# Performance work log

Hardware: AMD Instinct MI355X
Metric: run time of the kernel (lower is better)

Reference implementation:

```python
import jax, jax.numpy as jnp
import numpy as np

SEQ, B, I, H = 512, 64, 1024, 1024

def setup_inputs() -> dict:
    key = jax.random.key(0)
    ks = jax.random.split(key, 6)
    scale_ih = 1.0 / np.sqrt(I)
    scale_hh = 1.0 / np.sqrt(H)
    return {
        "input": jax.random.normal(ks[0], (SEQ, B, I), dtype=jnp.float32),
        "h_0": jax.random.normal(ks[1], (1, B, H), dtype=jnp.float32),
        "weight_ih": jax.random.normal(ks[2], (3 * H, I), dtype=jnp.float32) * scale_ih,
        "weight_hh": jax.random.normal(ks[3], (3 * H, H), dtype=jnp.float32) * scale_hh,
        "bias_ih": jax.random.normal(ks[4], (3 * H,), dtype=jnp.float32) * scale_hh,
        "bias_hh": jax.random.normal(ks[5], (3 * H,), dtype=jnp.float32) * scale_hh,
    }


def _gru_lbr0(input, h0, weight_ih, weight_hh, bias_ih, bias_hh):
    """Unidirectional GRU, ONNX linear_before_reset=0 semantics.

    r_t = sigmoid(x W_ir^T + b_ir + h W_hr^T + b_hr)
    z_t = sigmoid(x W_iz^T + b_iz + h W_hz^T + b_hz)
    n_t = tanh(x W_in^T + b_in + (r_t * h) W_hn^T + b_hn)
    h_t = (1 - z_t) * n_t + z_t * h
    """
    hidden = h0.shape[-1]
    # Precompute all input projections in one big GEMM: (S, B, 3H)
    gx = jnp.einsum('sbi,gi->sbg', input, weight_ih) + bias_ih
    W_hr, W_hz, W_hn = jnp.split(weight_hh, 3, axis=0)
    b_hr, b_hz, b_hn = jnp.split(bias_hh, 3, axis=0)

    def step(h, gx_t):
        gx_r, gx_z, gx_n = jnp.split(gx_t, 3, axis=-1)
        r = jax.nn.sigmoid(gx_r + h @ W_hr.T + b_hr)
        z = jax.nn.sigmoid(gx_z + h @ W_hz.T + b_hz)
        n = jnp.tanh(gx_n + (r * h) @ W_hn.T + b_hn)
        h_new = (1.0 - z) * n + z * h
        return h_new, h_new

    h_n, outputs = jax.lax.scan(step, h0, gx)
    return outputs, h_n  # (S, B, H), (B, H)


def reference(input, h_0, weight_ih, weight_hh, bias_ih, bias_hh):
    seq_len, batch, _ = input.shape
    hidden = weight_hh.shape[1]
    outputs, h_n = _gru_lbr0(input, h_0[0], weight_ih, weight_hh, bias_ih, bias_hh)
    # Match GRUWrapper output layout: Y = (S, num_dir=1, B, H), Y_h = (1, B, H)
    Y = outputs.reshape(seq_len, batch, 1, hidden).transpose(0, 2, 1, 3)
    Y_h = h_n[None, :, :]
    return (Y, Y_h)
```

## Files before the change

kernel.cpp:

```cpp
#include <hip/hip_runtime.h>

typedef unsigned short ushort_t;
typedef short sh8 __attribute__((ext_vector_type(8)));
typedef float f32x4 __attribute__((ext_vector_type(4)));

#define MFMA16(a,b,c) __builtin_amdgcn_mfma_f32_16x16x32_bf16((a),(b),(c),0,0,0)

#define SEQL   512
#define BATCH  64
#define HDIM   1024
#define G3     3072
#define AROWS  (SEQL*BATCH)
#define YSZ    (SEQL*BATCH*HDIM)
#define BH     (BATCH*HDIM)
#define NWG    64

__device__ __forceinline__ ushort_t f2bf(float x) {
  unsigned u = __float_as_uint(x);
  u += 0x7FFFu + ((u >> 16) & 1u);
  return (ushort_t)(u >> 16);
}
__device__ __forceinline__ float bf2f(ushort_t h) {
  return __uint_as_float(((unsigned)h) << 16);
}

__global__ void cvt_kernel(const float* __restrict__ wih, const float* __restrict__ whh,
                           const float* __restrict__ h0,
                           ushort_t* __restrict__ WihH, ushort_t* __restrict__ WihL,
                           ushort_t* __restrict__ WhhH, ushort_t* __restrict__ WhhL,
                           ushort_t* __restrict__ hH) {
  const int NW = G3 * HDIM;
  int i0 = blockIdx.x * blockDim.x + threadIdx.x;
  int stride = gridDim.x * blockDim.x;
  for (int i = i0; i < NW; i += stride) {
    float x = wih[i]; ushort_t h = f2bf(x);
    WihH[i] = h; WihL[i] = f2bf(x - bf2f(h));
    float y = whh[i]; ushort_t g = f2bf(y);
    WhhH[i] = g; WhhL[i] = f2bf(y - bf2f(g));
  }
  for (int i = i0; i < BH; i += stride) {
    hH[i] = f2bf(h0[i]);
  }
}

__global__ __launch_bounds__(256) void gemm_gx(
    const float* __restrict__ A,
    const ushort_t* __restrict__ BHp, const ushort_t* __restrict__ BLp,
    const float* __restrict__ bias,
    float* __restrict__ gx)
{
  int bid = blockIdx.x;
  int mt = bid / 24, nt = bid % 24;
  int w = threadIdx.x >> 6, l = threadIdx.x & 63;
  int lr = l & 15, lk = (l >> 4) * 8;

  f32x4 acc[2][8];
  #pragma unroll
  for (int mi = 0; mi < 2; ++mi)
    #pragma unroll
    for (int ni = 0; ni < 8; ++ni) acc[mi][ni] = (f32x4){0.f, 0.f, 0.f, 0.f};

  int arow0 = mt * 128 + w * 32 + lr;
  int brow0 = nt * 128 + lr;

  for (int k0 = 0; k0 < HDIM; k0 += 32) {
    int ka = k0 + lk;
    sh8 aH[2], aL[2];
    #pragma unroll
    for (int mi = 0; mi < 2; ++mi) {
      const float* ap = A + (size_t)(arow0 + mi * 16) * HDIM + ka;
      float4 x0 = *(const float4*)ap;
      float4 x1 = *(const float4*)(ap + 4);
      float xs[8] = {x0.x, x0.y, x0.z, x0.w, x1.x, x1.y, x1.z, x1.w};
      #pragma unroll
      for (int j = 0; j < 8; ++j) {
        ushort_t h = f2bf(xs[j]);
        aH[mi][j] = (short)h;
        aL[mi][j] = (short)f2bf(xs[j] - bf2f(h));
      }
    }
    #pragma unroll
    for (int ni = 0; ni < 8; ++ni) {
      const ushort_t* bh = BHp + (size_t)(brow0 + ni * 16) * HDIM + ka;
      const ushort_t* bl = BLp + (size_t)(brow0 + ni * 16) * HDIM + ka;
      sh8 bHf = *(const sh8*)bh;
      sh8 bLf = *(const sh8*)bl;
      #pragma unroll
      for (int mi = 0; mi < 2; ++mi) {
        acc[mi][ni] = MFMA16(aH[mi], bHf, acc[mi][ni]);
        acc[mi][ni] = MFMA16(aH[mi], bLf, acc[mi][ni]);
        acc[mi][ni] = MFMA16(aL[mi], bHf, acc[mi][ni]);
      }
    }
  }
  int rb = (l >> 4) * 4;
  #pragma unroll
  for (int mi = 0; mi < 2; ++mi)
    #pragma unroll
    for (int ni = 0; ni < 8; ++ni) {
      int col = nt * 128 + ni * 16 + lr;
      float b = bias[col];
      #pragma unroll
      for (int j = 0; j < 4; ++j) {
        int row = mt * 128 + w * 32 + mi * 16 + rb + j;
        __builtin_nontemporal_store(acc[mi][ni][j] + b, &gx[(size_t)row * G3 + col]);
      }
    }
}

__device__ __forceinline__ void gbar_flat(unsigned* slots, int g, int tid, unsigned e) {
  __syncthreads();
  if (tid < 64) {
    if (tid == 0)
      __hip_atomic_store(slots + g * 32, e, __ATOMIC_RELEASE, __HIP_MEMORY_SCOPE_AGENT);
    unsigned* sp = slots + tid * 32;
    while (__hip_atomic_load(sp, __ATOMIC_RELAXED, __HIP_MEMORY_SCOPE_AGENT) < e)
      __builtin_amdgcn_s_sleep(1);
    (void)__hip_atomic_load(sp, __ATOMIC_ACQUIRE, __HIP_MEMORY_SCOPE_AGENT);
  }
  __syncthreads();
}

__global__ __launch_bounds__(256, 1) void gru_rec(
    const float* __restrict__ gx,
    const ushort_t* __restrict__ WhhH, const ushort_t* __restrict__ WhhL,
    const float* __restrict__ bias_hh,
    const float* __restrict__ h0f,
    ushort_t* __restrict__ hH,
    ushort_t* __restrict__ rhH,
    float* __restrict__ Y, float* __restrict__ Yh,
    unsigned* __restrict__ slots)
{
  extern __shared__ char lds[];
  const int g = blockIdx.x;
  const int tid = threadIdx.x;
  const int w = tid >> 6, l = tid & 63;
  const int lr = l & 15, lk = (l >> 4) * 8, rb = (l >> 4) * 4;
  const int c0 = g * 16, m0 = w * 16;
  const int c = c0 + lr;

  #pragma unroll
  for (int p = 0; p < 32; ++p) {
    int q = tid + p * 256;
    int flat = q * 16;
    int lrow = flat >> 11;
    int off = flat & 2047;
    int dst = flat ^ ((lrow & 7) << 4);
    const ushort_t* src;
    if (lrow < 16)      src = WhhH + (size_t)(c0 + lrow) * HDIM;
    else if (lrow < 32) src = WhhH + (size_t)(1024 + c0 + lrow - 16) * HDIM;
    else if (lrow < 48) src = WhhH + (size_t)(2048 + c0 + lrow - 32) * HDIM;
    else                src = WhhL + (size_t)(2048 + c0 + lrow - 48) * HDIM;
    *(sh8*)(lds + dst) = *(const sh8*)(src + (off >> 1));
  }
  __syncthreads();

  const float br = bias_hh[c], bz = bias_hh[1024 + c], bn = bias_hh[2048 + c];
  unsigned bar = 0;

  float hold[4];
  #pragma unroll
  for (int j = 0; j < 4; ++j) hold[j] = h0f[(m0 + rb + j) * HDIM + c];

  float gxr[4], gxz[4], gxn[4];
  #pragma unroll
  for (int j = 0; j < 4; ++j) {
    int b = m0 + rb + j;
    gxr[j] = __builtin_nontemporal_load(gx + (size_t)b * G3 + c);
    gxz[j] = __builtin_nontemporal_load(gx + (size_t)b * G3 + 1024 + c);
    gxn[j] = __builtin_nontemporal_load(gx + (size_t)b * G3 + 2048 + c);
  }

  for (int t = 0; t < SEQL; ++t) {
    const int par = t & 1;

    const ushort_t* ha = hH + par * BH + (size_t)(m0 + lr) * HDIM + lk;
    sh8 bufa[32];
    #pragma unroll
    for (int i = 0; i < 32; ++i) bufa[i] = *(const sh8*)(ha + i * 32);

    f32x4 accR = (f32x4){0,0,0,0}, accZ = (f32x4){0,0,0,0};
    #pragma unroll
    for (int i = 0; i < 32; ++i) {
      int byt = ((lr << 11) + ((i * 32 + lk) << 1)) ^ ((lr & 7) << 4);
      sh8 rW = *(const sh8*)(lds + byt);
      sh8 zW = *(const sh8*)(lds + 32768 + byt);
      accR = MFMA16(bufa[i], rW, accR);
      accZ = MFMA16(bufa[i], zW, accZ);
    }

    float zreg[4];
    #pragma unroll
    for (int j = 0; j < 4; ++j) {
      int b = m0 + rb + j;
      float pr = accR[j] + gxr[j] + br;
      float pz = accZ[j] + gxz[j] + bz;
      float r = 1.f / (1.f + __expf(-pr));
      zreg[j] = 1.f / (1.f + __expf(-pz));
      rhH[b * HDIM + c] = f2bf(r * hold[j]);
    }
    ++bar;
    gbar_flat(slots, g, tid, bar);

    const ushort_t* ra = rhH + (size_t)(m0 + lr) * HDIM + lk;
    #pragma unroll
    for (int i = 0; i < 32; ++i) bufa[i] = *(const sh8*)(ra + i * 32);

    {
      int tn = (t + 1 < SEQL) ? t + 1 : t;
      const float* gxn2 = gx + (size_t)tn * (BATCH * G3);
      #pragma unroll
      for (int j = 0; j < 4; ++j) {
        int b = m0 + rb + j;
        gxr[j] = __builtin_nontemporal_load(gxn2 + (size_t)b * G3 + c);
        gxz[j] = __builtin_nontemporal_load(gxn2 + (size_t)b * G3 + 1024 + c);
      }
    }

    f32x4 accN = (f32x4){0,0,0,0};
    #pragma unroll
    for (int i = 0; i < 32; ++i) {
      int byt = ((lr << 11) + ((i * 32 + lk) << 1)) ^ ((lr & 7) << 4);
      sh8 nW = *(const sh8*)(lds + 65536 + byt);
      sh8 nLo = *(const sh8*)(lds + 98304 + byt);
      accN = MFMA16(bufa[i], nW, accN);
      accN = MFMA16(bufa[i], nLo, accN);
    }

    ushort_t* hHn = hH + (par ^ 1) * BH;
    float gxnN[4];
    {
      int tn = (t + 1 < SEQL) ? t + 1 : t;
      const float* gxn2 = gx + (size_t)tn * (BATCH * G3);
      #pragma unroll
      for (int j = 0; j < 4; ++j) {
        int b = m0 + rb + j;
        gxnN[j] = __builtin_nontemporal_load(gxn2 + (size_t)b * G3 + 2048 + c);
      }
    }
    #pragma unroll
    for (int j = 0; j < 4; ++j) {
      int b = m0 + rb + j;
      float pn = accN[j] + gxn[j] + bn;
      float n = tanhf(pn);
      float z = zreg[j];
      float hnew = (1.f - z) * n + z * hold[j];
      hold[j] = hnew;
      __builtin_nontemporal_store(hnew, &Y[(size_t)t * BH + b * HDIM + c]);
      hHn[b * HDIM + c] = f2bf(hnew);
      if (t == SEQL - 1) __builtin_nontemporal_store(hnew, &Yh[b * HDIM + c]);
    }
    #pragma unroll
    for (int j = 0; j < 4; ++j) gxn[j] = gxnN[j];

    if (t < SEQL - 1) {
      ++bar;
      gbar_flat(slots, g, tid, bar);
    }
  }
}

extern "C" void kernel_launch(void* const* d_in, const int* in_sizes, int n_in,
                              void* d_out, int out_size, void* d_ws, size_t ws_size,
                              hipStream_t stream) {
  const float* input = (const float*)d_in[0];
  const float* h0    = (const float*)d_in[1];
  const float* wih   = (const float*)d_in[2];
  const float* whh   = (const float*)d_in[3];
  const float* bih   = (const float*)d_in[4];
  const float* bhh   = (const float*)d_in[5];

  char* ws = (char*)d_ws;
  size_t o = 0;
  float* gx = (float*)(ws + o);         o += (size_t)AROWS * G3 * 4;
  ushort_t* WihH = (ushort_t*)(ws + o); o += (size_t)G3 * HDIM * 2;
  ushort_t* WihL = (ushort_t*)(ws + o); o += (size_t)G3 * HDIM * 2;
  ushort_t* WhhH = (ushort_t*)(ws + o); o += (size_t)G3 * HDIM * 2;
  ushort_t* WhhL = (ushort_t*)(ws + o); o += (size_t)G3 * HDIM * 2;
  ushort_t* hH = (ushort_t*)(ws + o);   o += 2 * (size_t)BH * 2;
  ushort_t* rhH = (ushort_t*)(ws + o);  o += (size_t)BH * 2;
  unsigned* slots = (unsigned*)(ws + o); o += (size_t)NWG * 128;

  float* Y  = (float*)d_out;
  float* Yh = (float*)d_out + (size_t)YSZ;

  (void)hipFuncSetAttribute((const void*)gru_rec,
                            hipFuncAttributeMaxDynamicSharedMemorySize, 131072);

  (void)hipMemsetAsync(slots, 0, (size_t)NWG * 128, stream);
  cvt_kernel<<<2048, 256, 0, stream>>>(wih, whh, h0, WihH, WihL, WhhH, WhhL, hH);
  gemm_gx<<<(AROWS / 128) * (G3 / 128), 256, 0, stream>>>(input, WihH, WihL, bih, gx);
  gru_rec<<<64, 256, 131072, stream>>>(gx, WhhH, WhhL, bhh, h0, hH, rhH, Y, Yh, slots);
}
```

Measured before the change: 8.765 ms.

## Replace acquire/release barrier with relaxed atomics on 32-bit-padded hidden state

```diff
diff --git a/kernel.cpp b/kernel.cpp
--- a/kernel.cpp
+++ b/kernel.cpp
@@ -28,7 +28,7 @@
                            const float* __restrict__ h0,
                            ushort_t* __restrict__ WihH, ushort_t* __restrict__ WihL,
                            ushort_t* __restrict__ WhhH, ushort_t* __restrict__ WhhL,
-                           ushort_t* __restrict__ hH) {
+                           unsigned* __restrict__ hU) {
   const int NW = G3 * HDIM;
   int i0 = blockIdx.x * blockDim.x + threadIdx.x;
   int stride = gridDim.x * blockDim.x;
@@ -39,7 +39,7 @@
     WhhH[i] = g; WhhL[i] = f2bf(y - bf2f(g));
   }
   for (int i = i0; i < BH; i += stride) {
-    hH[i] = f2bf(h0[i]);
+    hU[i] = (unsigned)f2bf(h0[i]);
   }
 }
 
@@ -108,28 +108,40 @@
     }
 }
 
-__device__ __forceinline__ void gbar_flat(unsigned* slots, int g, int tid, unsigned e) {
+__device__ __forceinline__ void gbar_nf(unsigned* slots, int g, int tid, unsigned e) {
   __syncthreads();
   if (tid < 64) {
     if (tid == 0)
-      __hip_atomic_store(slots + g * 32, e, __ATOMIC_RELEASE, __HIP_MEMORY_SCOPE_AGENT);
-    unsigned* sp = slots + tid * 32;
-    while (__hip_atomic_load(sp, __ATOMIC_RELAXED, __HIP_MEMORY_SCOPE_AGENT) < e)
+      __hip_atomic_store(slots + g, e, __ATOMIC_RELAXED, __HIP_MEMORY_SCOPE_AGENT);
+    while (__hip_atomic_load(slots + tid, __ATOMIC_RELAXED, __HIP_MEMORY_SCOPE_AGENT) < e)
       __builtin_amdgcn_s_sleep(1);
-    (void)__hip_atomic_load(sp, __ATOMIC_ACQUIRE, __HIP_MEMORY_SCOPE_AGENT);
   }
   __syncthreads();
 }
+
+#define LOADU(BUF_, base_) \
+  _Pragma("unroll") for (int i = 0; i < 32; ++i) { \
+    unsigned long long* p = (unsigned long long*)((base_) + i * 32); \
+    unsigned long long q0 = __hip_atomic_load(p + 0, __ATOMIC_RELAXED, __HIP_MEMORY_SCOPE_AGENT); \
+    unsigned long long q1 = __hip_atomic_load(p + 1, __ATOMIC_RELAXED, __HIP_MEMORY_SCOPE_AGENT); \
+    unsigned long long q2 = __hip_atomic_load(p + 2, __ATOMIC_RELAXED, __HIP_MEMORY_SCOPE_AGENT); \
+    unsigned long long q3 = __hip_atomic_load(p + 3, __ATOMIC_RELAXED, __HIP_MEMORY_SCOPE_AGENT); \
+    union { unsigned u[4]; sh8 s; } f_; \
+    f_.u[0] = (unsigned)q0 | ((unsigned)(q0 >> 32) << 16); \
+    f_.u[1] = (unsigned)q1 | ((unsigned)(q1 >> 32) << 16); \
+    f_.u[2] = (unsigned)q2 | ((unsigned)(q2 >> 32) << 16); \
+    f_.u[3] = (unsigned)q3 | ((unsigned)(q3 >> 32) << 16); \
+    BUF_[i] = f_.s; }
 
 __global__ __launch_bounds__(256, 1) void gru_rec(
     const float* __restrict__ gx,
     const ushort_t* __restrict__ WhhH, const ushort_t* __restrict__ WhhL,
     const float* __restrict__ bias_hh,
     const float* __restrict__ h0f,
-    ushort_t* __restrict__ hH,
-    ushort_t* __restrict__ rhH,
+    unsigned* hU,
+    unsigned* rhU,
     float* __restrict__ Y, float* __restrict__ Yh,
-    unsigned* __restrict__ slots)
+    unsigned* slots)
 {
   extern __shared__ char lds[];
   const int g = blockIdx.x;
@@ -174,10 +186,9 @@
   for (int t = 0; t < SEQL; ++t) {
     const int par = t & 1;
 
-    const ushort_t* ha = hH + par * BH + (size_t)(m0 + lr) * HDIM + lk;
+    unsigned* ha = hU + par * BH + (m0 + lr) * HDIM + lk;
     sh8 bufa[32];
-    #pragma unroll
-    for (int i = 0; i < 32; ++i) bufa[i] = *(const sh8*)(ha + i * 32);
+    LOADU(bufa, ha)
 
     f32x4 accR = (f32x4){0,0,0,0}, accZ = (f32x4){0,0,0,0};
     #pragma unroll
@@ -197,23 +208,23 @@
       float pz = accZ[j] + gxz[j] + bz;
       float r = 1.f / (1.f + __expf(-pr));
       zreg[j] = 1.f / (1.f + __expf(-pz));
-      rhH[b * HDIM + c] = f2bf(r * hold[j]);
+      __hip_atomic_store(rhU + b * HDIM + c, (unsigned)f2bf(r * hold[j]),
+                         __ATOMIC_RELAXED, __HIP_MEMORY_SCOPE_AGENT);
     }
     ++bar;
-    gbar_flat(slots, g, tid, bar);
-
-    const ushort_t* ra = rhH + (size_t)(m0 + lr) * HDIM + lk;
-    #pragma unroll
-    for (int i = 0; i < 32; ++i) bufa[i] = *(const sh8*)(ra + i * 32);
+    gbar_nf(slots, g, tid, bar);
+
+    unsigned* ra = rhU + (m0 + lr) * HDIM + lk;
+    LOADU(bufa, ra)
 
     {
       int tn = (t + 1 < SEQL) ? t + 1 : t;
-      const float* gxn2 = gx + (size_t)tn * (BATCH * G3);
+      const float* gxt1 = gx + (size_t)tn * (BATCH * G3);
       #pragma unroll
       for (int j = 0; j < 4; ++j) {
         int b = m0 + rb + j;
-        gxr[j] = __builtin_nontemporal_load(gxn2 + (size_t)b * G3 + c);
-        gxz[j] = __builtin_nontemporal_load(gxn2 + (size_t)b * G3 + 1024 + c);
+        gxr[j] = __builtin_nontemporal_load(gxt1 + (size_t)b * G3 + c);
+        gxz[j] = __builtin_nontemporal_load(gxt1 + (size_t)b * G3 + 1024 + c);
       }
     }
 
@@ -227,17 +238,18 @@
       accN = MFMA16(bufa[i], nLo, accN);
     }
 
-    ushort_t* hHn = hH + (par ^ 1) * BH;
     float gxnN[4];
     {
       int tn = (t + 1 < SEQL) ? t + 1 : t;
-      const float* gxn2 = gx + (size_t)tn * (BATCH * G3);
+      const float* gxt1 = gx + (size_t)tn * (BATCH * G3);
       #pragma unroll
       for (int j = 0; j < 4; ++j) {
         int b = m0 + rb + j;
-        gxnN[j] = __builtin_nontemporal_load(gxn2 + (size_t)b * G3 + 2048 + c);
-      }
-    }
+        gxnN[j] = __builtin_nontemporal_load(gxt1 + (size_t)b * G3 + 2048 + c);
+      }
+    }
+
+    unsigned* hUn = hU + (par ^ 1) * BH;
     #pragma unroll
     for (int j = 0; j < 4; ++j) {
       int b = m0 + rb + j;
@@ -246,16 +258,17 @@
       float z = zreg[j];
       float hnew = (1.f - z) * n + z * hold[j];
       hold[j] = hnew;
-      __builtin_nontemporal_store(hnew, &Y[(size_t)t * BH + b * HDIM + c]);
-      hHn[b * HDIM + c] = f2bf(hnew);
-      if (t == SEQL - 1) __builtin_nontemporal_store(hnew, &Yh[b * HDIM + c]);
+      Y[(size_t)t * BH + b * HDIM + c] = hnew;
+      __hip_atomic_store(hUn + b * HDIM + c, (unsigned)f2bf(hnew),
+                         __ATOMIC_RELAXED, __HIP_MEMORY_SCOPE_AGENT);
+      if (t == SEQL - 1) Yh[b * HDIM + c] = hnew;
     }
     #pragma unroll
     for (int j = 0; j < 4; ++j) gxn[j] = gxnN[j];
 
     if (t < SEQL - 1) {
       ++bar;
-      gbar_flat(slots, g, tid, bar);
+      gbar_nf(slots, g, tid, bar);
     }
   }
 }
@@ -277,9 +290,9 @@
   ushort_t* WihL = (ushort_t*)(ws + o); o += (size_t)G3 * HDIM * 2;
   ushort_t* WhhH = (ushort_t*)(ws + o); o += (size_t)G3 * HDIM * 2;
   ushort_t* WhhL = (ushort_t*)(ws + o); o += (size_t)G3 * HDIM * 2;
-  ushort_t* hH = (ushort_t*)(ws + o);   o += 2 * (size_t)BH * 2;
-  ushort_t* rhH = (ushort_t*)(ws + o);  o += (size_t)BH * 2;
-  unsigned* slots = (unsigned*)(ws + o); o += (size_t)NWG * 128;
+  unsigned* hU = (unsigned*)(ws + o);   o += 2 * (size_t)BH * 4;
+  unsigned* rhU = (unsigned*)(ws + o);  o += (size_t)BH * 4;
+  unsigned* slots = (unsigned*)(ws + o); o += 256;
 
   float* Y  = (float*)d_out;
   float* Yh = (float*)d_out + (size_t)YSZ;
@@ -287,8 +300,8 @@
   (void)hipFuncSetAttribute((const void*)gru_rec,
                             hipFuncAttributeMaxDynamicSharedMemorySize, 131072);
 
-  (void)hipMemsetAsync(slots, 0, (size_t)NWG * 128, stream);
-  cvt_kernel<<<2048, 256, 0, stream>>>(wih, whh, h0, WihH, WihL, WhhH, WhhL, hH);
+  (void)hipMemsetAsync(slots, 0, 256, stream);
+  cvt_kernel<<<2048, 256, 0, stream>>>(wih, whh, h0, WihH, WihL, WhhH, WhhL, hU);
   gemm_gx<<<(AROWS / 128) * (G3 / 128), 256, 0, stream>>>(input, WihH, WihL, bih, gx);
-  gru_rec<<<64, 256, 131072, stream>>>(gx, WhhH, WhhL, bhh, h0, hH, rhH, Y, Yh, slots);
-}
+  gru_rec<<<64, 256, 131072, stream>>>(gx, WhhH, WhhL, bhh, h0, hU, rhU, Y, Yh, slots);
+}
```

Result: slower. 20.18 ms (+130.2%).

## Fuse input GEMM and recurrence into one persistent kernel with progress flags

Applied to the files above, without the earlier changes.

```diff
diff --git a/kernel.cpp b/kernel.cpp
--- a/kernel.cpp
+++ b/kernel.cpp
@@ -14,6 +14,11 @@
 #define YSZ    (SEQL*BATCH*HDIM)
 #define BH     (BATCH*HDIM)
 #define NWG    64
+#define NGEMM  192
+#define NTILE  768
+
+#define TILES_TOTAL (256*24)
+#define TILES_PER_WG (TILES_TOTAL/NGEMM)
 
 __device__ __forceinline__ ushort_t f2bf(float x) {
   unsigned u = __float_as_uint(x);
@@ -43,71 +48,6 @@
   }
 }
 
-__global__ __launch_bounds__(256) void gemm_gx(
-    const float* __restrict__ A,
-    const ushort_t* __restrict__ BHp, const ushort_t* __restrict__ BLp,
-    const float* __restrict__ bias,
-    float* __restrict__ gx)
-{
-  int bid = blockIdx.x;
-  int mt = bid / 24, nt = bid % 24;
-  int w = threadIdx.x >> 6, l = threadIdx.x & 63;
-  int lr = l & 15, lk = (l >> 4) * 8;
-
-  f32x4 acc[2][8];
-  #pragma unroll
-  for (int mi = 0; mi < 2; ++mi)
-    #pragma unroll
-    for (int ni = 0; ni < 8; ++ni) acc[mi][ni] = (f32x4){0.f, 0.f, 0.f, 0.f};
-
-  int arow0 = mt * 128 + w * 32 + lr;
-  int brow0 = nt * 128 + lr;
-
-  for (int k0 = 0; k0 < HDIM; k0 += 32) {
-    int ka = k0 + lk;
-    sh8 aH[2], aL[2];
-    #pragma unroll
-    for (int mi = 0; mi < 2; ++mi) {
-      const float* ap = A + (size_t)(arow0 + mi * 16) * HDIM + ka;
-      float4 x0 = *(const float4*)ap;
-      float4 x1 = *(const float4*)(ap + 4);
-      float xs[8] = {x0.x, x0.y, x0.z, x0.w, x1.x, x1.y, x1.z, x1.w};
-      #pragma unroll
-      for (int j = 0; j < 8; ++j) {
-        ushort_t h = f2bf(xs[j]);
-        aH[mi][j] = (short)h;
-        aL[mi][j] = (short)f2bf(xs[j] - bf2f(h));
-      }
-    }
-    #pragma unroll
-    for (int ni = 0; ni < 8; ++ni) {
-      const ushort_t* bh = BHp + (size_t)(brow0 + ni * 16) * HDIM + ka;
-      const ushort_t* bl = BLp + (size_t)(brow0 + ni * 16) * HDIM + ka;
-      sh8 bHf = *(const sh8*)bh;
-      sh8 bLf = *(const sh8*)bl;
-      #pragma unroll
-      for (int mi = 0; mi < 2; ++mi) {
-        acc[mi][ni] = MFMA16(aH[mi], bHf, acc[mi][ni]);
-        acc[mi][ni] = MFMA16(aH[mi], bLf, acc[mi][ni]);
-        acc[mi][ni] = MFMA16(aL[mi], bHf, acc[mi][ni]);
-      }
-    }
-  }
-  int rb = (l >> 4) * 4;
-  #pragma unroll
-  for (int mi = 0; mi < 2; ++mi)
-    #pragma unroll
-    for (int ni = 0; ni < 8; ++ni) {
-      int col = nt * 128 + ni * 16 + lr;
-      float b = bias[col];
-      #pragma unroll
-      for (int j = 0; j < 4; ++j) {
-        int row = mt * 128 + w * 32 + mi * 16 + rb + j;
-        __builtin_nontemporal_store(acc[mi][ni][j] + b, &gx[(size_t)row * G3 + col]);
-      }
-    }
-}
-
 __device__ __forceinline__ void gbar_flat(unsigned* slots, int g, int tid, unsigned e) {
   __syncthreads();
   if (tid < 64) {
@@ -121,21 +61,91 @@
   __syncthreads();
 }
 
-__global__ __launch_bounds__(256, 1) void gru_rec(
-    const float* __restrict__ gx,
+__global__ __launch_bounds__(256, 1) void mega(
+    const float* __restrict__ A,
+    const ushort_t* __restrict__ WihH, const ushort_t* __restrict__ WihL,
+    const float* __restrict__ bih,
+    float* __restrict__ gx,
     const ushort_t* __restrict__ WhhH, const ushort_t* __restrict__ WhhL,
-    const float* __restrict__ bias_hh,
+    const float* __restrict__ bhh,
     const float* __restrict__ h0f,
     ushort_t* __restrict__ hH,
     ushort_t* __restrict__ rhH,
     float* __restrict__ Y, float* __restrict__ Yh,
-    unsigned* __restrict__ slots)
+    unsigned* __restrict__ slots,
+    unsigned* __restrict__ prog)
 {
   extern __shared__ char lds[];
   const int g = blockIdx.x;
   const int tid = threadIdx.x;
   const int w = tid >> 6, l = tid & 63;
   const int lr = l & 15, lk = (l >> 4) * 8, rb = (l >> 4) * 4;
+
+  if (g >= NWG) {
+    const int base = g - NWG;
+    for (int kk = 0; kk < TILES_PER_WG; ++kk) {
+      int tile = base + NGEMM * kk;
+      int mt = tile / 24, nt = tile % 24;
+
+      f32x4 acc[2][8];
+      #pragma unroll
+      for (int mi = 0; mi < 2; ++mi)
+        #pragma unroll
+        for (int ni = 0; ni < 8; ++ni) acc[mi][ni] = (f32x4){0.f, 0.f, 0.f, 0.f};
+
+      int arow0 = mt * 128 + w * 32 + lr;
+      int brow0 = nt * 128 + lr;
+
+      for (int k0 = 0; k0 < HDIM; k0 += 32) {
+        int ka = k0 + lk;
+        sh8 aH[2], aL[2];
+        #pragma unroll
+        for (int mi = 0; mi < 2; ++mi) {
+          const float* ap = A + (size_t)(arow0 + mi * 16) * HDIM + ka;
+          float4 x0 = *(const float4*)ap;
+          float4 x1 = *(const float4*)(ap + 4);
+          float xs[8] = {x0.x, x0.y, x0.z, x0.w, x1.x, x1.y, x1.z, x1.w};
+          #pragma unroll
+          for (int j = 0; j < 8; ++j) {
+            ushort_t h = f2bf(xs[j]);
+            aH[mi][j] = (short)h;
+            aL[mi][j] = (short)f2bf(xs[j] - bf2f(h));
+          }
+        }
+        #pragma unroll
+        for (int ni = 0; ni < 8; ++ni) {
+          const ushort_t* bh = WihH + (size_t)(brow0 + ni * 16) * HDIM + ka;
+          const ushort_t* bl = WihL + (size_t)(brow0 + ni * 16) * HDIM + ka;
+          sh8 bHf = *(const sh8*)bh;
+          sh8 bLf = *(const sh8*)bl;
+          #pragma unroll
+          for (int mi = 0; mi < 2; ++mi) {
+            acc[mi][ni] = MFMA16(aH[mi], bHf, acc[mi][ni]);
+            acc[mi][ni] = MFMA16(aH[mi], bLf, acc[mi][ni]);
+            acc[mi][ni] = MFMA16(aL[mi], bHf, acc[mi][ni]);
+          }
+        }
+      }
+      int rbq = (l >> 4) * 4;
+      #pragma unroll
+      for (int mi = 0; mi < 2; ++mi)
+        #pragma unroll
+        for (int ni = 0; ni < 8; ++ni) {
+          int col = nt * 128 + ni * 16 + lr;
+          float b = bih[col];
+          #pragma unroll
+          for (int j = 0; j < 4; ++j) {
+            int row = mt * 128 + w * 32 + mi * 16 + rbq + j;
+            __builtin_nontemporal_store(acc[mi][ni][j] + b, &gx[(size_t)row * G3 + col]);
+          }
+        }
+      __syncthreads();
+      if (tid == 0)
+        __hip_atomic_fetch_add(prog + mt, 1u, __ATOMIC_RELEASE, __HIP_MEMORY_SCOPE_AGENT);
+    }
+    return;
+  }
+
   const int c0 = g * 16, m0 = w * 16;
   const int c = c0 + lr;
 
@@ -155,13 +165,20 @@
   }
   __syncthreads();
 
-  const float br = bias_hh[c], bz = bias_hh[1024 + c], bn = bias_hh[2048 + c];
+  const float br = bhh[c], bz = bhh[1024 + c], bn = bhh[2048 + c];
   unsigned bar = 0;
+  int pready = 0;
 
   float hold[4];
   #pragma unroll
   for (int j = 0; j < 4; ++j) hold[j] = h0f[(m0 + rb + j) * HDIM + c];
 
+  {
+    while (__hip_atomic_load(prog, __ATOMIC_RELAXED, __HIP_MEMORY_SCOPE_AGENT) < 24u)
+      __builtin_amdgcn_s_sleep(1);
+    (void)__hip_atomic_load(prog, __ATOMIC_ACQUIRE, __HIP_MEMORY_SCOPE_AGENT);
+    pready = 1;
+  }
   float gxr[4], gxz[4], gxn[4];
   #pragma unroll
   for (int j = 0; j < 4; ++j) {
@@ -206,8 +223,15 @@
     #pragma unroll
     for (int i = 0; i < 32; ++i) bufa[i] = *(const sh8*)(ra + i * 32);
 
+    int tn = (t + 1 < SEQL) ? t + 1 : t;
     {
-      int tn = (t + 1 < SEQL) ? t + 1 : t;
+      int blk = tn >> 1;
+      if (blk >= pready) {
+        while (__hip_atomic_load(prog + blk, __ATOMIC_RELAXED, __HIP_MEMORY_SCOPE_AGENT) < 24u)
+          __builtin_amdgcn_s_sleep(1);
+        (void)__hip_atomic_load(prog + blk, __ATOMIC_ACQUIRE, __HIP_MEMORY_SCOPE_AGENT);
+        pready = blk + 1;
+      }
       const float* gxn2 = gx + (size_t)tn * (BATCH * G3);
       #pragma unroll
       for (int j = 0; j < 4; ++j) {
@@ -230,7 +254,6 @@
     ushort_t* hHn = hH + (par ^ 1) * BH;
     float gxnN[4];
     {
-      int tn = (t + 1 < SEQL) ? t + 1 : t;
       const float* gxn2 = gx + (size_t)tn * (BATCH * G3);
       #pragma unroll
       for (int j = 0; j < 4; ++j) {
@@ -280,15 +303,17 @@
   ushort_t* hH = (ushort_t*)(ws + o);   o += 2 * (size_t)BH * 2;
   ushort_t* rhH = (ushort_t*)(ws + o);  o += (size_t)BH * 2;
   unsigned* slots = (unsigned*)(ws + o); o += (size_t)NWG * 128;
+  unsigned* prog = (unsigned*)(ws + o);  o += 256 * 4;
 
   float* Y  = (float*)d_out;
   float* Yh = (float*)d_out + (size_t)YSZ;
 
-  (void)hipFuncSetAttribute((const void*)gru_rec,
+  (void)hipFuncSetAttribute((const void*)mega,
                             hipFuncAttributeMaxDynamicSharedMemorySize, 131072);
 
-  (void)hipMemsetAsync(slots, 0, (size_t)NWG * 128, stream);
+  (void)hipMemsetAsync(slots, 0, (size_t)NWG * 128 + 256 * 4, stream);
   cvt_kernel<<<2048, 256, 0, stream>>>(wih, whh, h0, WihH, WihL, WhhH, WhhL, hH);
-  gemm_gx<<<(AROWS / 128) * (G3 / 128), 256, 0, stream>>>(input, WihH, WihL, bih, gx);
-  gru_rec<<<64, 256, 131072, stream>>>(gx, WhhH, WhhL, bhh, h0, hH, rhH, Y, Yh, slots);
-}
+  mega<<<NWG + NGEMM, 256, 131072, stream>>>(input, WihH, WihL, bih, gx,
+                                             WhhH, WhhL, bhh, h0, hH, rhH,
+                                             Y, Yh, slots, prog);
+}
```

After: 8.682 ms. Within noise of the previous version (-0.9%).

## Replace acquire/release grid barrier with sc1 loads/stores and fuse Whh conversion

Applied to the files above, without the earlier changes.

```diff
diff --git a/kernel.cpp b/kernel.cpp
--- a/kernel.cpp
+++ b/kernel.cpp
@@ -24,10 +24,13 @@
   return __uint_as_float(((unsigned)h) << 16);
 }
 
-__global__ void cvt_kernel(const float* __restrict__ wih, const float* __restrict__ whh,
-                           const float* __restrict__ h0,
+#define LOAD16_SC1(dst, p) \
+  asm volatile("global_load_dwordx4 %0, %1, off sc1" : "=v"(dst) : "v"(p) : "memory")
+#define STORE16_SC1(p, v) \
+  asm volatile("global_store_short %0, %1, off sc1" :: "v"(p), "v"(v) : "memory")
+
+__global__ void cvt_kernel(const float* __restrict__ wih, const float* __restrict__ h0,
                            ushort_t* __restrict__ WihH, ushort_t* __restrict__ WihL,
-                           ushort_t* __restrict__ WhhH, ushort_t* __restrict__ WhhL,
                            ushort_t* __restrict__ hH) {
   const int NW = G3 * HDIM;
   int i0 = blockIdx.x * blockDim.x + threadIdx.x;
@@ -35,8 +38,6 @@
   for (int i = i0; i < NW; i += stride) {
     float x = wih[i]; ushort_t h = f2bf(x);
     WihH[i] = h; WihL[i] = f2bf(x - bf2f(h));
-    float y = whh[i]; ushort_t g = f2bf(y);
-    WhhH[i] = g; WhhL[i] = f2bf(y - bf2f(g));
   }
   for (int i = i0; i < BH; i += stride) {
     hH[i] = f2bf(h0[i]);
@@ -108,23 +109,30 @@
     }
 }
 
-__device__ __forceinline__ void gbar_flat(unsigned* slots, int g, int tid, unsigned e) {
+__device__ __forceinline__ void gbar_nf(unsigned* slots, int g, int tid, unsigned e) {
+  asm volatile("s_waitcnt vmcnt(0)" ::: "memory");
   __syncthreads();
   if (tid < 64) {
     if (tid == 0)
-      __hip_atomic_store(slots + g * 32, e, __ATOMIC_RELEASE, __HIP_MEMORY_SCOPE_AGENT);
+      __hip_atomic_store(slots + g * 32, e, __ATOMIC_RELAXED, __HIP_MEMORY_SCOPE_AGENT);
     unsigned* sp = slots + tid * 32;
     while (__hip_atomic_load(sp, __ATOMIC_RELAXED, __HIP_MEMORY_SCOPE_AGENT) < e)
       __builtin_amdgcn_s_sleep(1);
-    (void)__hip_atomic_load(sp, __ATOMIC_ACQUIRE, __HIP_MEMORY_SCOPE_AGENT);
   }
   __syncthreads();
 }
+
+#define LOAD_BURST_SC1(BUF_, base_) \
+  _Pragma("unroll") for (int i = 0; i < 32; ++i) { \
+    LOAD16_SC1(BUF_[i], (const void*)((base_) + i * 32)); \
+  } \
+  asm volatile("s_waitcnt vmcnt(0)" ::: "memory"); \
+  __builtin_amdgcn_sched_barrier(0);
 
 __global__ __launch_bounds__(256, 1) void gru_rec(
     const float* __restrict__ gx,
-    const ushort_t* __restrict__ WhhH, const ushort_t* __restrict__ WhhL,
-    const float* __restrict__ bias_hh,
+    const float* __restrict__ whh,
+    const float* __restrict__ bhh,
     const float* __restrict__ h0f,
     ushort_t* __restrict__ hH,
     ushort_t* __restrict__ rhH,
@@ -146,16 +154,27 @@
     int lrow = flat >> 11;
     int off = flat & 2047;
     int dst = flat ^ ((lrow & 7) << 4);
-    const ushort_t* src;
-    if (lrow < 16)      src = WhhH + (size_t)(c0 + lrow) * HDIM;
-    else if (lrow < 32) src = WhhH + (size_t)(1024 + c0 + lrow - 16) * HDIM;
-    else if (lrow < 48) src = WhhH + (size_t)(2048 + c0 + lrow - 32) * HDIM;
-    else                src = WhhL + (size_t)(2048 + c0 + lrow - 48) * HDIM;
-    *(sh8*)(lds + dst) = *(const sh8*)(src + (off >> 1));
+    int col = off >> 1;
+    const float* src;
+    bool lo = false;
+    if (lrow < 16)      src = whh + (size_t)(c0 + lrow) * HDIM + col;
+    else if (lrow < 32) src = whh + (size_t)(1024 + c0 + lrow - 16) * HDIM + col;
+    else if (lrow < 48) src = whh + (size_t)(2048 + c0 + lrow - 32) * HDIM + col;
+    else              { src = whh + (size_t)(2048 + c0 + lrow - 48) * HDIM + col; lo = true; }
+    float4 x0 = *(const float4*)src;
+    float4 x1 = *(const float4*)(src + 4);
+    float xs[8] = {x0.x, x0.y, x0.z, x0.w, x1.x, x1.y, x1.z, x1.w};
+    union { ushort_t v[8]; sh8 s; } pk;
+    #pragma unroll
+    for (int j = 0; j < 8; ++j) {
+      ushort_t hi = f2bf(xs[j]);
+      pk.v[j] = lo ? f2bf(xs[j] - bf2f(hi)) : hi;
+    }
+    *(sh8*)(lds + dst) = pk.s;
   }
   __syncthreads();
 
-  const float br = bias_hh[c], bz = bias_hh[1024 + c], bn = bias_hh[2048 + c];
+  const float br = bhh[c], bz = bhh[1024 + c], bn = bhh[2048 + c];
   unsigned bar = 0;
 
   float hold[4];
@@ -175,9 +194,8 @@
     const int par = t & 1;
 
     const ushort_t* ha = hH + par * BH + (size_t)(m0 + lr) * HDIM + lk;
-    sh8 bufa[32];
-    #pragma unroll
-    for (int i = 0; i < 32; ++i) bufa[i] = *(const sh8*)(ha + i * 32);
+    f32x4 raw[32];
+    LOAD_BURST_SC1(raw, ha)
 
     f32x4 accR = (f32x4){0,0,0,0}, accZ = (f32x4){0,0,0,0};
     #pragma unroll
@@ -185,8 +203,9 @@
       int byt = ((lr << 11) + ((i * 32 + lk) << 1)) ^ ((lr & 7) << 4);
       sh8 rW = *(const sh8*)(lds + byt);
       sh8 zW = *(const sh8*)(lds + 32768 + byt);
-      accR = MFMA16(bufa[i], rW, accR);
-      accZ = MFMA16(bufa[i], zW, accZ);
+      sh8 av = __builtin_bit_cast(sh8, raw[i]);
+      accR = MFMA16(av, rW, accR);
+      accZ = MFMA16(av, zW, accZ);
     }
 
     float zreg[4];
@@ -197,17 +216,17 @@
       float pz = accZ[j] + gxz[j] + bz;
       float r = 1.f / (1.f + __expf(-pr));
       zreg[j] = 1.f / (1.f + __expf(-pz));
-      rhH[b * HDIM + c] = f2bf(r * hold[j]);
+      unsigned v = (unsigned)f2bf(r * hold[j]);
+      STORE16_SC1((void*)(rhH + b * HDIM + c), v);
     }
     ++bar;
-    gbar_flat(slots, g, tid, bar);
+    gbar_nf(slots, g, tid, bar);
 
     const ushort_t* ra = rhH + (size_t)(m0 + lr) * HDIM + lk;
-    #pragma unroll
-    for (int i = 0; i < 32; ++i) bufa[i] = *(const sh8*)(ra + i * 32);
-
+    LOAD_BURST_SC1(raw, ra)
+
+    int tn = (t + 1 < SEQL) ? t + 1 : t;
     {
-      int tn = (t + 1 < SEQL) ? t + 1 : t;
       const float* gxn2 = gx + (size_t)tn * (BATCH * G3);
       #pragma unroll
       for (int j = 0; j < 4; ++j) {
@@ -223,14 +242,14 @@
       int byt = ((lr << 11) + ((i * 32 + lk) << 1)) ^ ((lr & 7) << 4);
       sh8 nW = *(const sh8*)(lds + 65536 + byt);
       sh8 nLo = *(const sh8*)(lds + 98304 + byt);
-      accN = MFMA16(bufa[i], nW, accN);
-      accN = MFMA16(bufa[i], nLo, accN);
+      sh8 av = __builtin_bit_cast(sh8, raw[i]);
+      accN = MFMA16(av, nW, accN);
+      accN = MFMA16(av, nLo, accN);
     }
 
     ushort_t* hHn = hH + (par ^ 1) * BH;
     float gxnN[4];
     {
-      int tn = (t + 1 < SEQL) ? t + 1 : t;
       const float* gxn2 = gx + (size_t)tn * (BATCH * G3);
       #pragma unroll
       for (int j = 0; j < 4; ++j) {
@@ -246,16 +265,17 @@
       float z = zreg[j];
       float hnew = (1.f - z) * n + z * hold[j];
       hold[j] = hnew;
-      __builtin_nontemporal_store(hnew, &Y[(size_t)t * BH + b * HDIM + c]);
-      hHn[b * HDIM + c] = f2bf(hnew);
-      if (t == SEQL - 1) __builtin_nontemporal_store(hnew, &Yh[b * HDIM + c]);
+      Y[(size_t)t * BH + b * HDIM + c] = hnew;
+      unsigned v = (unsigned)f2bf(hnew);
+      STORE16_SC1((void*)(hHn + b * HDIM + c), v);
+      if (t == SEQL - 1) Yh[b * HDIM + c] = hnew;
     }
     #pragma unroll
     for (int j = 0; j < 4; ++j) gxn[j] = gxnN[j];
 
     if (t < SEQL - 1) {
       ++bar;
-      gbar_flat(slots, g, tid, bar);
+      gbar_nf(slots, g, tid, bar);
     }
   }
 }
@@ -275,8 +295,6 @@
   float* gx = (float*)(ws + o);         o += (size_t)AROWS * G3 * 4;
   ushort_t* WihH = (ushort_t*)(ws + o); o += (size_t)G3 * HDIM * 2;
   ushort_t* WihL = (ushort_t*)(ws + o); o += (size_t)G3 * HDIM * 2;
-  ushort_t* WhhH = (ushort_t*)(ws + o); o += (size_t)G3 * HDIM * 2;
-  ushort_t* WhhL = (ushort_t*)(ws + o); o += (size_t)G3 * HDIM * 2;
   ushort_t* hH = (ushort_t*)(ws + o);   o += 2 * (size_t)BH * 2;
   ushort_t* rhH = (ushort_t*)(ws + o);  o += (size_t)BH * 2;
   unsigned* slots = (unsigned*)(ws + o); o += (size_t)NWG * 128;
@@ -288,7 +306,7 @@
                             hipFuncAttributeMaxDynamicSharedMemorySize, 131072);
 
   (void)hipMemsetAsync(slots, 0, (size_t)NWG * 128, stream);
-  cvt_kernel<<<2048, 256, 0, stream>>>(wih, whh, h0, WihH, WihL, WhhH, WhhL, hH);
+  cvt_kernel<<<2048, 256, 0, stream>>>(wih, h0, WihH, WihL, hH);
   gemm_gx<<<(AROWS / 128) * (G3 / 128), 256, 0, stream>>>(input, WihH, WihL, bih, gx);
-  gru_rec<<<64, 256, 131072, stream>>>(gx, WhhH, WhhL, bhh, h0, hH, rhH, Y, Yh, slots);
-}
+  gru_rec<<<64, 256, 131072, stream>>>(gx, whh, bhh, h0, hH, rhH, Y, Yh, slots);
+}
```

New measurement: 8.990 ms. 2.6% more time.
